# Kernel tuning notes

Hardware: AMD Instinct MI355X
Metric: run time of the kernel (lower is better)

The kernel has to match this reference:

```python
import jax, jax.numpy as jnp
import numpy as np

N = 8192
E = 262144
DIN = 512
DOUT = 256


def setup_inputs() -> dict:
    key = jax.random.key(0)
    k1, k2, k3, k4 = jax.random.split(key, 4)
    x = jax.random.normal(k1, (N, DIN), dtype=jnp.float32)
    edge_index = jax.random.randint(k2, (2, E), 0, N, dtype=jnp.int64)
    edge_weight = jax.random.uniform(k3, (E,), dtype=jnp.float32)
    W = jax.random.normal(k4, (DOUT, DIN), dtype=jnp.float32) * (1.0 / np.sqrt(DIN))
    return {"x": x, "edge_index": edge_index, "edge_weight": edge_weight, "W": W}


def reference(x, edge_index, edge_weight, W):
    n = x.shape[0]
    # Linear(dim_in, dim_out, bias=False): h = x @ W.T  -> [N, DOUT]
    h = x @ W.T
    # Dense adjacency: A[src, dst] += w (to_dense_adj sums duplicate edges)
    src, dst = edge_index[0], edge_index[1]
    A = jnp.zeros((n, n), dtype=x.dtype).at[src, dst].add(edge_weight)
    # degree from A BEFORE self-loops, then +1 from the added eye on degree_matrix
    deg = jnp.sum(A, axis=1) + 1.0
    # sqrt(inverse(diag(deg))) == diag(1/sqrt(deg)); apply as row scaling
    dinv_sqrt = 1.0 / jnp.sqrt(deg)  # [N]
    A = A + jnp.eye(n, dtype=x.dtype)  # self-loops on adjacency
    # x = D^{-1/2} @ (A.T @ (D^{-1/2} @ h))
    h = dinv_sqrt[:, None] * h
    h = A.T @ h
    h = dinv_sqrt[:, None] * h
    return h
```

## Files before the change

### kernel.cpp

```cpp
#include <hip/hip_runtime.h>

static constexpr int DIN = 512;
static constexpr int DOUT = 256;
static constexpr int NB = 64;
static constexpr int SLOT = 12;
static constexpr int NNODE = 8192;
static constexpr int LCAP = 256;
static constexpr float DEG_SCALE = 1048576.0f;
static constexpr float DEG_INV = 1.0f / 1048576.0f;

typedef __attribute__((ext_vector_type(8))) short short8;
typedef __attribute__((ext_vector_type(4))) float f32x4;
typedef __attribute__((ext_vector_type(2))) unsigned int u32x2;
typedef __attribute__((ext_vector_type(4))) unsigned int u32x4;

__device__ inline unsigned short f2bf(float f) {
  unsigned int b = __float_as_uint(f);
  unsigned int r = (b + 0x7fffu + ((b >> 16) & 1u)) >> 16;
  return (unsigned short)r;
}
__device__ inline float bf_lo(unsigned int packed) { return __uint_as_float(packed << 16); }
__device__ inline float bf_hi(unsigned int packed) { return __uint_as_float(packed & 0xffff0000u); }

__device__ inline short8 cvt8(const f32x4 a, const f32x4 b) {
  short8 o;
  o[0] = (short)f2bf(a[0]); o[1] = (short)f2bf(a[1]);
  o[2] = (short)f2bf(a[2]); o[3] = (short)f2bf(a[3]);
  o[4] = (short)f2bf(b[0]); o[5] = (short)f2bf(b[1]);
  o[6] = (short)f2bf(b[2]); o[7] = (short)f2bf(b[3]);
  return o;
}

__global__ __launch_bounds__(256) void k_binprep(
    const int* __restrict__ ei, const float* __restrict__ ew,
    const float* __restrict__ W, unsigned short* __restrict__ wbb,
    int* __restrict__ cnt_rep, int* __restrict__ deg_rep,
    u32x2* __restrict__ bucket, int E) {
  if (blockIdx.x < NB) {
    __shared__ int s_cnt[NNODE];
    __shared__ int s_deg[NNODE];
    const int b = blockIdx.x;
    const int t = threadIdx.x;
    for (int i = t; i < NNODE; i += 256) { s_cnt[i] = 0; s_deg[i] = 0; }
    __syncthreads();
    const int base = b * (E / NB);
    const int iters = (E / NB) / 256;
    for (int i = 0; i < iters; ++i) {
      const int e = base + i * 256 + t;
      int sv = __builtin_nontemporal_load(ei + e);
      int dv = __builtin_nontemporal_load(ei + E + e);
      float w = __builtin_nontemporal_load(ew + e);
      atomicAdd(&s_cnt[dv], 1);
      atomicAdd(&s_deg[sv], __float2int_rn(w * DEG_SCALE));
    }
    __syncthreads();
    for (int i = t; i < NNODE; i += 256) {
      cnt_rep[b * NNODE + i] = s_cnt[i];
      deg_rep[b * NNODE + i] = s_deg[i];
    }
    __syncthreads();
    for (int i = t; i < NNODE; i += 256) s_cnt[i] = 0;
    __syncthreads();
    for (int i = 0; i < iters; ++i) {
      const int e = base + i * 256 + t;
      int sv = __builtin_nontemporal_load(ei + e);
      int dv = __builtin_nontemporal_load(ei + E + e);
      float w = __builtin_nontemporal_load(ew + e);
      int r = atomicAdd(&s_cnt[dv], 1);
      if (r < SLOT) {
        u32x2 v;
        v[0] = (unsigned)sv;
        v[1] = __float_as_uint(w);
        __builtin_nontemporal_store(
            v, bucket + ((size_t)dv * SLOT + r) * NB + b);
      }
    }
  } else {
    const int gid = (blockIdx.x - NB) * 256 + threadIdx.x;
    const f32x4* src = (const f32x4*)(W + (size_t)gid * 8);
    f32x4 a = src[0], bb = src[1];
    *(short8*)(wbb + (size_t)gid * 8) = cvt8(a, bb);
  }
}

__global__ __launch_bounds__(256) void k_gemm(
    const float* __restrict__ x, const unsigned short* __restrict__ wbb,
    const int* __restrict__ deg_rep, float* __restrict__ sdeg,
    unsigned short* __restrict__ h1b, int n) {
  if (blockIdx.x < (n >> 8)) {
    const int i = blockIdx.x * 256 + threadIdx.x;
    int sum = 0;
#pragma unroll
    for (int r = 0; r < NB; ++r) sum += deg_rep[r * NNODE + i];
    sdeg[i] = __frsqrt_rn(1.0f + (float)sum * DEG_INV);
  }
  const int lane = threadIdx.x & 63;
  const int wv = threadIdx.x >> 6;
  const int bm = blockIdx.x * 16;
  const int colb = wv * 64;
  const int r = lane & 15;
  const int kg = lane >> 4;
  f32x4 acc[4] = {};
  const float* arow = x + (size_t)(bm + r) * DIN + kg * 8;
  const unsigned short* brow0 = wbb + (size_t)(colb + r) * DIN + kg * 8;
#pragma unroll
  for (int k0 = 0; k0 < DIN; k0 += 32) {
    f32x4 a0 = *(const f32x4*)(arow + k0);
    f32x4 a1 = *(const f32x4*)(arow + k0 + 4);
    short8 av = cvt8(a0, a1);
#pragma unroll
    for (int nt = 0; nt < 4; ++nt) {
      short8 bv = *(const short8*)(brow0 + (size_t)nt * 16 * DIN + k0);
      acc[nt] = __builtin_amdgcn_mfma_f32_16x16x32_bf16(av, bv, acc[nt], 0, 0, 0);
    }
  }
#pragma unroll
  for (int i = 0; i < 4; ++i) {
    int row = bm + kg * 4 + i;
#pragma unroll
    for (int nt = 0; nt < 4; ++nt) {
      h1b[(size_t)row * DOUT + colb + nt * 16 + r] = f2bf(acc[nt][i]);
    }
  }
}

__global__ __launch_bounds__(256, 4) void k_gather(
    const unsigned short* __restrict__ h1b, const float* __restrict__ sdeg,
    const int* __restrict__ cnt_rep, const u32x2* __restrict__ bucket,
    float* __restrict__ out, int n) {
  __shared__ u32x2 s_edge[4][LCAP];
  const int lane = threadIdx.x & 63;
  const int wv = threadIdx.x >> 6;
  const int dst = blockIdx.x * 4 + wv;
  const int cl = lane & 31;
  const int half = lane >> 5;

  int c = min(cnt_rep[lane * NNODE + dst], SLOT);
  int inc = c;
#pragma unroll
  for (int d = 1; d < 64; d <<= 1) {
    int v = __shfl_up(inc, d);
    if (lane >= d) inc += v;
  }
  const int p = inc - c;
  int cnt = __shfl(inc, 63);
  int maxc = c;
#pragma unroll
  for (int d = 32; d; d >>= 1) maxc = max(maxc, __shfl_xor(maxc, d));

  for (int j = 0; j < maxc; ++j) {
    if (j < c && p + j < LCAP) {
      s_edge[wv][p + j] =
          __builtin_nontemporal_load(bucket + ((size_t)dst * SLOT + j) * NB + lane);
    }
  }
  cnt = min(cnt, LCAP);

  const u32x4 selfv = *(const u32x4*)(h1b + (size_t)dst * DOUT + cl * 8);
  const float sd = sdeg[dst];

  __syncthreads();

  float acc[8] = {};
  for (int base = 0; base < cnt; base += 64) {
    const int cc = min(64, cnt - base);
    int sv = 0;
    float wl = 0.f;
    if (lane < cc) {
      u32x2 ev = s_edge[wv][base + lane];
      sv = (int)ev[0];
      wl = __uint_as_float(ev[1]) * sdeg[sv];
    }
    const int npair = ((cc + 15) >> 4) << 3;
    for (int j = 0; j < npair; j += 8) {
      u32x4 rbuf[8];
#pragma unroll
      for (int u = 0; u < 8; ++u) {
        int src = __shfl(sv, 2 * (j + u) + half);
        rbuf[u] = *(const u32x4*)(h1b + (size_t)src * DOUT + cl * 8);
      }
#pragma unroll
      for (int u = 0; u < 8; ++u) {
        float w = __shfl(wl, 2 * (j + u) + half);
        acc[0] = fmaf(w, bf_lo(rbuf[u][0]), acc[0]);
        acc[1] = fmaf(w, bf_hi(rbuf[u][0]), acc[1]);
        acc[2] = fmaf(w, bf_lo(rbuf[u][1]), acc[2]);
        acc[3] = fmaf(w, bf_hi(rbuf[u][1]), acc[3]);
        acc[4] = fmaf(w, bf_lo(rbuf[u][2]), acc[4]);
        acc[5] = fmaf(w, bf_hi(rbuf[u][2]), acc[5]);
        acc[6] = fmaf(w, bf_lo(rbuf[u][3]), acc[6]);
        acc[7] = fmaf(w, bf_hi(rbuf[u][3]), acc[7]);
      }
    }
  }

#pragma unroll
  for (int k = 0; k < 8; ++k) acc[k] += __shfl_xor(acc[k], 32);

  if (half == 0) {
    f32x4 o0v, o1v;
    o0v[0] = sd * fmaf(sd, bf_lo(selfv[0]), acc[0]);
    o0v[1] = sd * fmaf(sd, bf_hi(selfv[0]), acc[1]);
    o0v[2] = sd * fmaf(sd, bf_lo(selfv[1]), acc[2]);
    o0v[3] = sd * fmaf(sd, bf_hi(selfv[1]), acc[3]);
    o1v[0] = sd * fmaf(sd, bf_lo(selfv[2]), acc[4]);
    o1v[1] = sd * fmaf(sd, bf_hi(selfv[2]), acc[5]);
    o1v[2] = sd * fmaf(sd, bf_lo(selfv[3]), acc[6]);
    o1v[3] = sd * fmaf(sd, bf_hi(selfv[3]), acc[7]);
    float* op = out + (size_t)dst * DOUT + cl * 8;
    __builtin_nontemporal_store(o0v, (f32x4*)op);
    __builtin_nontemporal_store(o1v, (f32x4*)(op + 4));
  }
}

extern "C" void kernel_launch(void* const* d_in, const int* in_sizes, int n_in,
                              void* d_out, int out_size, void* d_ws, size_t ws_size,
                              hipStream_t stream) {
  const float* x = (const float*)d_in[0];
  const int* ei = (const int*)d_in[1];
  const float* ew = (const float*)d_in[2];
  const float* W = (const float*)d_in[3];
  float* out = (float*)d_out;

  const int n = in_sizes[0] / DIN;
  const int E = in_sizes[2];

  char* p = (char*)d_ws;
  auto alloc = [&](size_t bytes) {
    char* q = p;
    p += (bytes + 255) & ~(size_t)255;
    return q;
  };
  unsigned short* h1b = (unsigned short*)alloc((size_t)n * DOUT * 2);
  unsigned short* wbb = (unsigned short*)alloc((size_t)DOUT * DIN * 2);
  int* cnt_rep = (int*)alloc((size_t)NB * NNODE * 4);
  int* deg_rep = (int*)alloc((size_t)NB * NNODE * 4);
  float* sdeg  = (float*)alloc((size_t)n * 4);
  u32x2* bucket = (u32x2*)alloc((size_t)n * SLOT * NB * 8);

  const int WCVT_BLOCKS = (DOUT * DIN / 8) / 256;

  k_binprep<<<NB + WCVT_BLOCKS, 256, 0, stream>>>(ei, ew, W, wbb, cnt_rep,
                                                  deg_rep, bucket, E);
  k_gemm<<<n / 16, 256, 0, stream>>>(x, wbb, deg_rep, sdeg, h1b, n);
  k_gather<<<n / 4, 256, 0, stream>>>(h1b, sdeg, cnt_rep, bucket, out, n);
}
```

Measured before the change: 82.69 us.

## Move bucket-fill pass out of histogram kernel to run alongside GEMM

The second edge pass (slot assignment and bucket scatter) is moved from the histogram kernel into a combined middle kernel. There it runs as separate blocks next to the degree reduction and the GEMM blocks. This shortens the 64-block histogram kernel, which occupies few CUs, and lets the scatter overlap with GEMM work. The cost is that edge indices are read again and the shared-memory count array is rebuilt in the new kernel. The GEMM blocks now also carry a 32KB static shared allocation, which may lower their occupancy.

```diff
diff --git a/kernel.cpp b/kernel.cpp
--- a/kernel.cpp
+++ b/kernel.cpp
@@ -31,11 +31,10 @@
   return o;
 }
 
-__global__ __launch_bounds__(256) void k_binprep(
+__global__ __launch_bounds__(256) void k_hist(
     const int* __restrict__ ei, const float* __restrict__ ew,
     const float* __restrict__ W, unsigned short* __restrict__ wbb,
-    int* __restrict__ cnt_rep, int* __restrict__ deg_rep,
-    u32x2* __restrict__ bucket, int E) {
+    int* __restrict__ cnt_rep, int* __restrict__ deg_rep, int E) {
   if (blockIdx.x < NB) {
     __shared__ int s_cnt[NNODE];
     __shared__ int s_deg[NNODE];
@@ -58,9 +57,36 @@
       cnt_rep[b * NNODE + i] = s_cnt[i];
       deg_rep[b * NNODE + i] = s_deg[i];
     }
-    __syncthreads();
+  } else {
+    const int gid = (blockIdx.x - NB) * 256 + threadIdx.x;
+    const f32x4* src = (const f32x4*)(W + (size_t)gid * 8);
+    f32x4 a = src[0], bb = src[1];
+    *(short8*)(wbb + (size_t)gid * 8) = cvt8(a, bb);
+  }
+}
+
+__global__ __launch_bounds__(256) void k_mid(
+    const int* __restrict__ ei, const float* __restrict__ ew,
+    const float* __restrict__ x, const unsigned short* __restrict__ wbb,
+    const int* __restrict__ deg_rep, float* __restrict__ sdeg,
+    u32x2* __restrict__ bucket, unsigned short* __restrict__ h1b, int E) {
+  __shared__ int s_cnt[NNODE];
+  const int blk = blockIdx.x;
+  if (blk < 32) {
+    const int i = blk * 256 + threadIdx.x;
+    int sum = 0;
+#pragma unroll
+    for (int r = 0; r < NB; ++r) sum += deg_rep[r * NNODE + i];
+    sdeg[i] = __frsqrt_rn(1.0f + (float)sum * DEG_INV);
+    return;
+  }
+  if (blk < 32 + NB) {
+    const int b = blk - 32;
+    const int t = threadIdx.x;
     for (int i = t; i < NNODE; i += 256) s_cnt[i] = 0;
     __syncthreads();
+    const int base = b * (E / NB);
+    const int iters = (E / NB) / 256;
     for (int i = 0; i < iters; ++i) {
       const int e = base + i * 256 + t;
       int sv = __builtin_nontemporal_load(ei + e);
@@ -71,32 +97,15 @@
         u32x2 v;
         v[0] = (unsigned)sv;
         v[1] = __float_as_uint(w);
-        __builtin_nontemporal_store(
-            v, bucket + ((size_t)dv * SLOT + r) * NB + b);
+        __builtin_nontemporal_store(v, bucket + ((size_t)dv * SLOT + r) * NB + b);
       }
     }
-  } else {
-    const int gid = (blockIdx.x - NB) * 256 + threadIdx.x;
-    const f32x4* src = (const f32x4*)(W + (size_t)gid * 8);
-    f32x4 a = src[0], bb = src[1];
-    *(short8*)(wbb + (size_t)gid * 8) = cvt8(a, bb);
-  }
-}
-
-__global__ __launch_bounds__(256) void k_gemm(
-    const float* __restrict__ x, const unsigned short* __restrict__ wbb,
-    const int* __restrict__ deg_rep, float* __restrict__ sdeg,
-    unsigned short* __restrict__ h1b, int n) {
-  if (blockIdx.x < (n >> 8)) {
-    const int i = blockIdx.x * 256 + threadIdx.x;
-    int sum = 0;
-#pragma unroll
-    for (int r = 0; r < NB; ++r) sum += deg_rep[r * NNODE + i];
-    sdeg[i] = __frsqrt_rn(1.0f + (float)sum * DEG_INV);
-  }
+    return;
+  }
+  const int g = blk - 32 - NB;
   const int lane = threadIdx.x & 63;
   const int wv = threadIdx.x >> 6;
-  const int bm = blockIdx.x * 16;
+  const int bm = g * 16;
   const int colb = wv * 64;
   const int r = lane & 15;
   const int kg = lane >> 4;
@@ -239,9 +248,11 @@
   u32x2* bucket = (u32x2*)alloc((size_t)n * SLOT * NB * 8);
 
   const int WCVT_BLOCKS = (DOUT * DIN / 8) / 256;
-
-  k_binprep<<<NB + WCVT_BLOCKS, 256, 0, stream>>>(ei, ew, W, wbb, cnt_rep,
-                                                  deg_rep, bucket, E);
-  k_gemm<<<n / 16, 256, 0, stream>>>(x, wbb, deg_rep, sdeg, h1b, n);
+  const int GB = n / 16;
+
+  k_hist<<<NB + WCVT_BLOCKS, 256, 0, stream>>>(ei, ew, W, wbb, cnt_rep,
+                                               deg_rep, E);
+  k_mid<<<32 + NB + GB, 256, 0, stream>>>(ei, ew, x, wbb, deg_rep, sdeg,
+                                          bucket, h1b, E);
   k_gather<<<n / 4, 256, 0, stream>>>(h1b, sdeg, cnt_rep, bucket, out, n);
 }
```

After: 72.92 us. -11.8%, faster.
